# Kernel optimization log

Hardware: AMD Instinct MI355X
Metric: run time of the kernel (lower is better)

Reference implementation:

```python
import jax, jax.numpy as jnp
import numpy as np

B, L, C = 8, 4096, 256
H = 8            # num_heads
D = C // H       # head_dim = 32
CHUNK = 128


def _build_slopes(n):
    # ALiBi slopes for power-of-2 n: 2^(-8/n * (i+1)); cast fp16 like the torch module
    s = np.array([2.0 ** (-(8.0 / n) * (i + 1)) for i in range(n)], dtype=np.float32)
    return jnp.asarray(s.astype(np.float16).astype(np.float32))  # [H]


def setup_inputs() -> dict:
    key = jax.random.key(0)
    ks = jax.random.split(key, 6)
    x = jax.random.normal(ks[0], (B, L, C), dtype=jnp.float32)
    rel_pos = jax.random.normal(ks[1], (1, L, C), dtype=jnp.float32) * 0.02  # trunc_normal std=0.02
    qkv_w = jax.random.normal(ks[2], (3 * C, C), dtype=jnp.float32) * (C ** -0.5)
    q_gamma = jnp.ones((H, 1, D), dtype=jnp.float32) / (D ** 0.5)
    k_gamma = jnp.ones((H, 1, D), dtype=jnp.float32) / (D ** 0.5)
    proj_w = jax.random.normal(ks[3], (C, C), dtype=jnp.float32) * (C ** -0.5)
    proj_b = jnp.zeros((C,), dtype=jnp.float32)
    return {"x": x, "rel_pos": rel_pos, "qkv_w": qkv_w, "q_gamma": q_gamma,
            "k_gamma": k_gamma, "proj_w": proj_w, "proj_b": proj_b}


def _rms_norm(t, gamma):
    # t: [B,H,L,D]; gamma: [H,1,D]. F.normalize(dim=-1) then * sqrt(D) * gamma
    n = jnp.sqrt(jnp.sum(t * t, axis=-1, keepdims=True))
    t = t / jnp.maximum(n, 1e-12)
    return t * (D ** 0.5) * gamma[None]


def _lightning_attn(q, k, v, slopes):
    # q,k,v: [B,H,L,D]; slopes: [H]. o_t = sum_{s<=t} exp(-slope*(t-s)) (q_t.k_s) v_s
    nc = L // CHUNK
    c = CHUNK
    qc = q.reshape(B, H, nc, c, D)
    kc = k.reshape(B, H, nc, c, D)
    vc = v.reshape(B, H, nc, c, D)

    idx = jnp.arange(c, dtype=jnp.float32)
    diff = idx[:, None] - idx[None, :]                       # [c,c]
    s = slopes[:, None, None]                                # [H,1,1]
    mask = jnp.where(diff >= 0, jnp.exp(-s * diff), 0.0)     # [H,c,c]

    # intra-chunk: [B,H,nc,c,c]
    scores = jnp.einsum("bhncd,bhnmd->bhncm", qc, kc) * mask[None, :, None]
    o_intra = jnp.einsum("bhncm,bhnmd->bhncd", scores, vc)

    # inter-chunk recurrence over decayed KV state [B,H,D,D]
    q_decay = jnp.exp(-slopes[:, None] * idx[None, :])[None, :, :, None]        # [1,H,c,1]
    k_decay = jnp.exp(-slopes[:, None] * (c - idx[None, :]))[None, :, :, None]  # [1,H,c,1]
    blk_decay = jnp.exp(-slopes * c)[:, None, None]                             # [H,1,1]

    def step(kv, inp):
        qi, ki, vi = inp                                   # each [B,H,c,D]
        o = jnp.einsum("bhcd,bhde->bhce", qi * q_decay, kv)
        kv = blk_decay * kv + jnp.einsum("bhcd,bhce->bhde", ki * k_decay, vi)
        return kv, o

    kv0 = jnp.zeros((B, H, D, D), dtype=q.dtype)
    qs = jnp.moveaxis(qc, 2, 0)  # [nc,B,H,c,D]
    ks_ = jnp.moveaxis(kc, 2, 0)
    vs = jnp.moveaxis(vc, 2, 0)
    _, o_inter = jax.lax.scan(step, kv0, (qs, ks_, vs))    # [nc,B,H,c,D]
    o_inter = jnp.moveaxis(o_inter, 0, 2)                  # [B,H,nc,c,D]

    return (o_intra + o_inter).reshape(B, H, L, D)


def reference(x, rel_pos, qkv_w, q_gamma, k_gamma, proj_w, proj_b):
    slopes = _build_slopes(H)
    h = x + rel_pos                                        # [B,L,C]
    qkv = h @ qkv_w.T                                      # [B,L,3C]
    qkv = qkv.reshape(B, L, 3, H, D).transpose(2, 0, 3, 1, 4)  # [3,B,H,L,D]
    q, k, v = qkv[0], qkv[1], qkv[2]
    q = q * (D ** -0.5)            # no-op through normalize, kept for fidelity
    q = _rms_norm(q, q_gamma)
    k = _rms_norm(k, k_gamma)
    o = _lightning_attn(q, k, v, slopes)                   # [B,H,L,D]
    o = o.transpose(0, 2, 1, 3).reshape(B, L, C)
    return o @ proj_w.T + proj_b
```

## Files before the change

kernel.cpp:

```cpp
#include <hip/hip_runtime.h>
#include <hip/hip_bf16.h>

#define B_ 8
#define L_ 4096
#define C_ 256
#define H_ 8
#define D_ 32
#define CHUNK_ 128
#define NC_ 32
#define M_ (B_*L_)

typedef _Float16 f16x8 __attribute__((ext_vector_type(8)));
typedef _Float16 f16x4 __attribute__((ext_vector_type(4)));
typedef float    f32x4 __attribute__((ext_vector_type(4)));

#define GLOAD_LDS16(g, l) __builtin_amdgcn_global_load_lds( \
    (const __attribute__((address_space(1))) unsigned int*)(g), \
    (__attribute__((address_space(3))) unsigned int*)(l), 16, 0, 0)

__global__ __launch_bounds__(256) void k_cast_w(
    const float* __restrict__ qw, const float* __restrict__ pw,
    _Float16* __restrict__ qwb, _Float16* __restrict__ pwb)
{
    const int i = (blockIdx.x * 256 + threadIdx.x) * 4;
    const float* src; _Float16* dst; int off;
    if (i < 768 * 256) { src = qw; dst = qwb; off = i; }
    else               { src = pw; dst = pwb; off = i - 768 * 256; }
    float4 v = *(const float4*)(src + off);
    f16x4 o = { (_Float16)v.x, (_Float16)v.y, (_Float16)v.z, (_Float16)v.w };
    *(f16x4*)(dst + off) = o;
}

__global__ __launch_bounds__(512) void k_qkv_fused(
    const float* __restrict__ x, const float* __restrict__ rel,
    const _Float16* __restrict__ Bw,
    const float* __restrict__ qg, const float* __restrict__ kg,
    _Float16* __restrict__ Qg, _Float16* __restrict__ Kg, _Float16* __restrict__ Vtg)
{
    __shared__ __align__(16) char smem[24576];
    _Float16* As = (_Float16*)smem;
    _Float16* Bs = As + 128 * 32;
    _Float16* Ws = (_Float16*)smem;

    const int tid = threadIdx.x;
    const int wv = tid >> 6, ln = tid & 63;
    const int kind = blockIdx.x;
    const int m0 = blockIdx.y * 128;
    const int wr = wv >> 1, wc = wv & 1;
    const int lr = ln >> 2, lc = (ln & 3) * 8;
    const int fr = ln & 15, fk = (ln >> 4) * 8;

    const int arow = tid >> 2;
    const int aseg = (tid & 3) * 8;
    const float* xp = x   + (size_t)(m0 + arow) * 256 + aseg;
    const float* rp = rel + (size_t)((m0 + arow) & 4095) * 256 + aseg;
    const _Float16* gb = Bw + (size_t)(kind * 256 + wv * 16 + lr) * 256 + lc;

    f32x4 acc[2][8] = {};
    for (int k0 = 0; k0 < 256; k0 += 32) {
        GLOAD_LDS16(gb + k0,             Bs + (wv * 16) * 32);
        GLOAD_LDS16(gb + k0 + 128 * 256, Bs + (128 + wv * 16) * 32);
        float4 x0 = *(const float4*)(xp + k0);
        float4 x1 = *(const float4*)(xp + k0 + 4);
        float4 r0 = *(const float4*)(rp + k0);
        float4 r1 = *(const float4*)(rp + k0 + 4);
        f16x8 hv = { (_Float16)(x0.x + r0.x), (_Float16)(x0.y + r0.y),
                     (_Float16)(x0.z + r0.z), (_Float16)(x0.w + r0.w),
                     (_Float16)(x1.x + r1.x), (_Float16)(x1.y + r1.y),
                     (_Float16)(x1.z + r1.z), (_Float16)(x1.w + r1.w) };
        *(f16x8*)(As + arow * 32 + aseg) = hv;
        __syncthreads();
        f16x8 af[2], bf[8];
#pragma unroll
        for (int i = 0; i < 2; ++i)
            af[i] = *(const f16x8*)(As + (wr * 32 + i * 16 + fr) * 32 + fk);
#pragma unroll
        for (int j = 0; j < 8; ++j)
            bf[j] = *(const f16x8*)(Bs + (wc * 128 + j * 16 + fr) * 32 + fk);
#pragma unroll
        for (int i = 0; i < 2; ++i)
#pragma unroll
            for (int j = 0; j < 8; ++j)
                acc[i][j] = __builtin_amdgcn_mfma_f32_16x16x32_f16(
                    af[i], bf[j], acc[i][j], 0, 0, 0);
        __syncthreads();
    }

    const int cr = (ln >> 4) * 4, cc = ln & 15;
    const int bb = m0 >> 12, l00 = m0 & 4095;

    if (kind < 2) {
        const float* gsrc = kind ? kg : qg;
        _Float16* P = kind ? Kg : Qg;
#pragma unroll
        for (int p = 0; p < 4; ++p) {
            const int h = wc * 4 + p;
            const float g0 = gsrc[h * 32 + cc];
            const float g1 = gsrc[h * 32 + 16 + cc];
#pragma unroll
            for (int i = 0; i < 2; ++i)
#pragma unroll
                for (int r = 0; r < 4; ++r) {
                    const float a0 = acc[i][2 * p][r];
                    const float a1 = acc[i][2 * p + 1][r];
                    float ss = a0 * a0 + a1 * a1;
                    ss += __shfl_xor(ss, 1);
                    ss += __shfl_xor(ss, 2);
                    ss += __shfl_xor(ss, 4);
                    ss += __shfl_xor(ss, 8);
                    const float sc = 5.656854249492381f / fmaxf(sqrtf(ss), 1e-12f);
                    const int row = wr * 32 + i * 16 + cr + r;
                    Ws[row * 72 + wc * 32 + cc]      = (_Float16)(a0 * sc * g0);
                    Ws[row * 72 + wc * 32 + 16 + cc] = (_Float16)(a1 * sc * g1);
                }
            __syncthreads();
            const int half = tid >> 8;
            const int t = tid & 255;
            const int hh = half * 4 + p;
            _Float16* dst = P + ((size_t)(bb * 8 + hh) * 4096 + l00) * 32;
#pragma unroll
            for (int cidx = 0; cidx < 2; ++cidx) {
                const int c = t + cidx * 256;
                const int rr = c >> 2, part = (c & 3) * 8;
                f16x8 v8 = *(const f16x8*)(Ws + rr * 72 + half * 32 + part);
                *(f16x8*)(dst + rr * 32 + part) = v8;
            }
            __syncthreads();
        }
    } else {
#pragma unroll
        for (int i = 0; i < 2; ++i)
#pragma unroll
            for (int j = 0; j < 8; ++j) {
                const int col = wc * 128 + j * 16 + cc;
                const int hh = col >> 5, e = col & 31;
                const int l0 = l00 + wr * 32 + i * 16 + cr;
                f16x4 v4 = { (_Float16)acc[i][j][0], (_Float16)acc[i][j][1],
                             (_Float16)acc[i][j][2], (_Float16)acc[i][j][3] };
                *(f16x4*)(Vtg + ((size_t)(bb * 8 + hh) * 32 + e) * 4096 + l0) = v4;
            }
    }
}

__global__ __launch_bounds__(256) void k_chunk_kv(
    const _Float16* __restrict__ Kg, const _Float16* __restrict__ Vtg,
    float* __restrict__ kvbuf)
{
    __shared__ float ks[128 * 32];
    __shared__ float vs[128 * 36];
    const int blk = blockIdx.x;
    const int n  = blk & 31;
    const int bh = blk >> 5;
    const int h  = bh & 7;
    const float sl2 = exp2f(-(float)(h + 1)) * 1.44269504f;
    const int tid = threadIdx.x;
    const _Float16* Kc = Kg + ((size_t)bh * 4096 + n * CHUNK_) * 32;
#pragma unroll
    for (int i = 0; i < 2; ++i) {
        const int flat = i * 256 + tid;
        const int pos = flat >> 2, d0 = (flat & 3) * 8;
        f16x8 k8 = *(const f16x8*)(Kc + flat * 8);
        const float kd = exp2f(-sl2 * (float)(CHUNK_ - pos));
        f32x4 lo = { (float)k8[0] * kd, (float)k8[1] * kd, (float)k8[2] * kd, (float)k8[3] * kd };
        f32x4 hi = { (float)k8[4] * kd, (float)k8[5] * kd, (float)k8[6] * kd, (float)k8[7] * kd };
        *(f32x4*)&ks[pos * 32 + d0]     = lo;
        *(f32x4*)&ks[pos * 32 + d0 + 4] = hi;
        const int e = flat >> 4, seg = flat & 15;
        f16x8 v8 = *(const f16x8*)(Vtg + ((size_t)bh * 32 + e) * 4096 + n * CHUNK_ + seg * 8);
#pragma unroll
        for (int j = 0; j < 8; ++j) vs[(seg * 8 + j) * 36 + e] = (float)v8[j];
    }
    __syncthreads();
    const int d = tid >> 3;
    const int e0 = (tid & 7) * 4;
    f32x4 acc = {0.f, 0.f, 0.f, 0.f};
    for (int pos = 0; pos < CHUNK_; ++pos) {
        const float kd = ks[pos * 32 + d];
        f32x4 v4 = *(const f32x4*)&vs[pos * 36 + e0];
        acc += kd * v4;
    }
    *(f32x4*)(kvbuf + (size_t)blk * 1024 + d * 32 + e0) = acc;
}

__global__ __launch_bounds__(256) void k_scan(float* __restrict__ kvbuf)
{
    const int bh = blockIdx.x;
    const int tid = threadIdx.x;
    const float slope = exp2f(-(float)((bh & 7) + 1));
    const float bd = __expf(-slope * (float)CHUNK_);
    float4 st = {0.f, 0.f, 0.f, 0.f};
    float4* base = (float4*)(kvbuf + (size_t)bh * NC_ * 1024) + tid;
#pragma unroll
    for (int g = 0; g < 4; ++g) {
        float4 tmp[8];
#pragma unroll
        for (int k = 0; k < 8; ++k) tmp[k] = base[(g * 8 + k) * 256];
#pragma unroll
        for (int k = 0; k < 8; ++k) {
            base[(g * 8 + k) * 256] = st;
            st.x = bd * st.x + tmp[k].x;
            st.y = bd * st.y + tmp[k].y;
            st.z = bd * st.z + tmp[k].z;
            st.w = bd * st.w + tmp[k].w;
        }
    }
}

__global__ __launch_bounds__(256) void k_attn(
    const _Float16* __restrict__ Qg, const _Float16* __restrict__ Kg,
    const _Float16* __restrict__ Vtg, const float* __restrict__ kvbuf,
    _Float16* __restrict__ attnp)
{
    __shared__ _Float16 Qs[128 * 32];
    __shared__ _Float16 Ks[128 * 32];
    __shared__ _Float16 Vt[32 * 136];
    __shared__ _Float16 KVt[32 * 40];
    __shared__ _Float16 Ss[128 * 136];
    __shared__ _Float16 Os[128 * 36];
    __shared__ float ejs[CHUNK_];
    const int blk = blockIdx.x;
    const int n  = blk & 31;
    const int bh = blk >> 5;
    const int h  = bh & 7;
    const float sl2 = exp2f(-(float)(h + 1)) * 1.44269504f;
    const int tid = threadIdx.x;
    const int wv = tid >> 6, ln = tid & 63;

    const _Float16* Qc = Qg + ((size_t)bh * 4096 + n * CHUNK_) * 32;
    const _Float16* Kc = Kg + ((size_t)bh * 4096 + n * CHUNK_) * 32;
#pragma unroll
    for (int i = 0; i < 2; ++i) {
        GLOAD_LDS16(Qc + (wv * 128 + i * 64 + ln) * 8, Qs + (wv * 128 + i * 64) * 8);
        GLOAD_LDS16(Kc + (wv * 128 + i * 64 + ln) * 8, Ks + (wv * 128 + i * 64) * 8);
    }
#pragma unroll
    for (int i = 0; i < 2; ++i) {
        int flat = i * 256 + tid;
        int e = flat >> 4, seg = flat & 15;
        f16x8 v8 = *(const f16x8*)(Vtg + ((size_t)bh * 32 + e) * 4096 + n * CHUNK_ + seg * 8);
        *(f16x8*)(Vt + e * 136 + seg * 8) = v8;
    }
    {
        int e = tid & 31, dg = tid >> 5;
        const float* kvp = kvbuf + (size_t)blk * 1024;
        f16x4 kv4 = { (_Float16)kvp[(dg * 4 + 0) * 32 + e],
                      (_Float16)kvp[(dg * 4 + 1) * 32 + e],
                      (_Float16)kvp[(dg * 4 + 2) * 32 + e],
                      (_Float16)kvp[(dg * 4 + 3) * 32 + e] };
        *(f16x4*)(KVt + e * 40 + dg * 4) = kv4;
    }
    if (tid < CHUNK_) ejs[tid] = exp2f(sl2 * (float)tid);
    __syncthreads();

    const int fr = ln & 15, fk = (ln >> 4) * 8;
    const int cr = (ln >> 4) * 4, cc = ln & 15;

    f16x8 aq[2];
#pragma unroll
    for (int i = 0; i < 2; ++i)
        aq[i] = *(const f16x8*)(Qs + (wv * 32 + i * 16 + fr) * 32 + fk);

    f32x4 sacc[2][8] = {};
#pragma unroll
    for (int j = 0; j < 8; ++j) {
        f16x8 bk = *(const f16x8*)(Ks + (j * 16 + fr) * 32 + fk);
#pragma unroll
        for (int i = 0; i < 2; ++i)
            sacc[i][j] = __builtin_amdgcn_mfma_f32_16x16x32_f16(aq[i], bk, sacc[i][j], 0, 0, 0);
    }
    f32x4 iacc[2][2] = {};
#pragma unroll
    for (int ct = 0; ct < 2; ++ct) {
        f16x8 bkv = *(const f16x8*)(KVt + (ct * 16 + fr) * 40 + fk);
#pragma unroll
        for (int i = 0; i < 2; ++i)
            iacc[i][ct] = __builtin_amdgcn_mfma_f32_16x16x32_f16(aq[i], bkv, iacc[i][ct], 0, 0, 0);
    }
    float ejr[8];
#pragma unroll
    for (int j = 0; j < 8; ++j) ejr[j] = ejs[j * 16 + cc];
    const float c1 = exp2f(-sl2);
    float qd_save[2][4];
#pragma unroll
    for (int i = 0; i < 2; ++i) {
        float er = exp2f(-sl2 * (float)(wv * 32 + i * 16 + cr));
#pragma unroll
        for (int r = 0; r < 4; ++r) {
            const int irow = wv * 32 + i * 16 + cr + r;
            qd_save[i][r] = er;
#pragma unroll
            for (int j = 0; j < 8; ++j) {
                const int jcol = j * 16 + cc;
                const float w = (jcol <= irow) ? ejr[j] * er : 0.f;
                Ss[irow * 136 + jcol] = (_Float16)(sacc[i][j][r] * w);
            }
            er *= c1;
        }
    }
    __syncthreads();

    f32x4 oacc[2][2] = {};
#pragma unroll
    for (int k = 0; k < 4; ++k) {
        f16x8 as[2], bv[2];
#pragma unroll
        for (int i = 0; i < 2; ++i)
            as[i] = *(const f16x8*)(Ss + (wv * 32 + i * 16 + fr) * 136 + k * 32 + fk);
#pragma unroll
        for (int ct = 0; ct < 2; ++ct)
            bv[ct] = *(const f16x8*)(Vt + (ct * 16 + fr) * 136 + k * 32 + fk);
#pragma unroll
        for (int i = 0; i < 2; ++i)
#pragma unroll
            for (int ct = 0; ct < 2; ++ct)
                oacc[i][ct] = __builtin_amdgcn_mfma_f32_16x16x32_f16(as[i], bv[ct], oacc[i][ct], 0, 0, 0);
    }
#pragma unroll
    for (int i = 0; i < 2; ++i)
#pragma unroll
        for (int r = 0; r < 4; ++r) {
            const int irow = wv * 32 + i * 16 + cr + r;
            const float qd = qd_save[i][r];
            Os[irow * 36 + cc]      = (_Float16)(oacc[i][0][r] + qd * iacc[i][0][r]);
            Os[irow * 36 + 16 + cc] = (_Float16)(oacc[i][1][r] + qd * iacc[i][1][r]);
        }
    __syncthreads();
    _Float16* abase = attnp + ((size_t)bh * 4096 + n * CHUNK_) * 32;
#pragma unroll
    for (int kk = 0; kk < 2; ++kk) {
        const int c = kk * 256 + tid;
        const int rr = c >> 2;
        const int part = (c & 3) * 8;
        *(f16x8*)(abase + rr * 32 + part) = *(const f16x8*)(Os + rr * 36 + part);
    }
}

__global__ __launch_bounds__(256) void k_proj_gemm(
    const _Float16* __restrict__ attnp, const _Float16* __restrict__ Bw,
    const float* __restrict__ bias, float* __restrict__ Cc)
{
    __shared__ _Float16 As[128 * 32];
    __shared__ _Float16 Bs[128 * 32];
    const int tid = threadIdx.x;
    const int wv = tid >> 6, ln = tid & 63;
    const int m0 = blockIdx.y * 128;
    const int n0 = blockIdx.x * 128;
    const int lr = ln >> 2;
    const int lc = (ln & 3) * 8;
    const int wm = (wv >> 1) * 64;
    const int wn = (wv & 1) * 64;
    const int fr = ln & 15;
    const int fk = (ln >> 4) * 8;

    f32x4 acc[4][4] = {};
    const int gmrow = m0 + wv * 16 + lr;
    const _Float16* ga = attnp +
        ((size_t)(gmrow >> 12) * 8 * 4096 + (gmrow & 4095)) * 32 + lc;
    const _Float16* gb = Bw + (size_t)(n0 + wv * 16 + lr) * 256 + lc;

    for (int k0 = 0; k0 < 256; k0 += 32) {
        const size_t hoff = (size_t)(k0 >> 5) * (4096 * 32);
        GLOAD_LDS16(ga + hoff,           As + (wv * 16) * 32);
        GLOAD_LDS16(ga + hoff + 64 * 32, As + (64 + wv * 16) * 32);
        GLOAD_LDS16(gb + k0,             Bs + (wv * 16) * 32);
        GLOAD_LDS16(gb + k0 + 64 * 256,  Bs + (64 + wv * 16) * 32);
        __syncthreads();
        f16x8 af[4], bf[4];
#pragma unroll
        for (int i = 0; i < 4; ++i)
            af[i] = *(const f16x8*)(As + (wm + i * 16 + fr) * 32 + fk);
#pragma unroll
        for (int j = 0; j < 4; ++j)
            bf[j] = *(const f16x8*)(Bs + (wn + j * 16 + fr) * 32 + fk);
#pragma unroll
        for (int i = 0; i < 4; ++i)
#pragma unroll
            for (int j = 0; j < 4; ++j)
                acc[i][j] = __builtin_amdgcn_mfma_f32_16x16x32_f16(
                    af[i], bf[j], acc[i][j], 0, 0, 0);
        __syncthreads();
    }
    const int cr = (ln >> 4) * 4;
    const int cc = ln & 15;
#pragma unroll
    for (int i = 0; i < 4; ++i)
#pragma unroll
        for (int j = 0; j < 4; ++j) {
            const int row = m0 + wm + i * 16 + cr;
            const int col = n0 + wn + j * 16 + cc;
            float* cp = Cc + (size_t)row * 256 + col;
            const float bb = bias[col];
#pragma unroll
            for (int r = 0; r < 4; ++r) cp[(size_t)r * 256] = acc[i][j][r] + bb;
        }
}

extern "C" void kernel_launch(void* const* d_in, const int* in_sizes, int n_in,
                              void* d_out, int out_size, void* d_ws, size_t ws_size,
                              hipStream_t stream)
{
    const float* x     = (const float*)d_in[0];
    const float* rel   = (const float*)d_in[1];
    const float* qkv_w = (const float*)d_in[2];
    const float* qg    = (const float*)d_in[3];
    const float* kg    = (const float*)d_in[4];
    const float* pw    = (const float*)d_in[5];
    const float* pb    = (const float*)d_in[6];
    float* out = (float*)d_out;
    char* wsb = (char*)d_ws;

    float*    kvb   = (float*)wsb;
    _Float16* Qg    = (_Float16*)(wsb + ((size_t)8  << 20));
    _Float16* Kg    = (_Float16*)(wsb + ((size_t)24 << 20));
    _Float16* Vtg   = (_Float16*)(wsb + ((size_t)40 << 20));
    _Float16* attnp = (_Float16*)(wsb + ((size_t)56 << 20));
    _Float16* qwb   = (_Float16*)(wsb + ((size_t)72 << 20));
    _Float16* pwb   = (_Float16*)(wsb + ((size_t)73 << 20));

    k_cast_w<<<256, 256, 0, stream>>>(qkv_w, pw, qwb, pwb);
    k_qkv_fused<<<dim3(3, 256), 512, 0, stream>>>(x, rel, qwb, qg, kg, Qg, Kg, Vtg);
    k_chunk_kv<<<2048, 256, 0, stream>>>(Kg, Vtg, kvb);
    k_scan<<<64, 256, 0, stream>>>(kvb);
    k_attn<<<2048, 256, 0, stream>>>(Qg, Kg, Vtg, kvb, attnp);
    k_proj_gemm<<<dim3(2, 256), 256, 0, stream>>>(attnp, pwb, pb, out);
}
```

Baseline: 203.4 us.

## Split x+rel cast into own kernel, retile QKV GEMM, read attn operands from global

Result: faster. 188.3 us (-7.4%).

```diff
diff --git a/kernel.cpp b/kernel.cpp
--- a/kernel.cpp
+++ b/kernel.cpp
@@ -18,6 +18,22 @@
     (const __attribute__((address_space(1))) unsigned int*)(g), \
     (__attribute__((address_space(3))) unsigned int*)(l), 16, 0, 0)
 
+__global__ __launch_bounds__(256) void k_cast_h(
+    const float* __restrict__ x, const float* __restrict__ rel, _Float16* __restrict__ h)
+{
+    const int i = (blockIdx.x * 256 + threadIdx.x) * 8;
+    float4 x0 = *(const float4*)(x + i);
+    float4 x1 = *(const float4*)(x + i + 4);
+    const int ri = i & (L_ * C_ - 1);
+    float4 r0 = *(const float4*)(rel + ri);
+    float4 r1 = *(const float4*)(rel + ri + 4);
+    f16x8 o = { (_Float16)(x0.x + r0.x), (_Float16)(x0.y + r0.y),
+                (_Float16)(x0.z + r0.z), (_Float16)(x0.w + r0.w),
+                (_Float16)(x1.x + r1.x), (_Float16)(x1.y + r1.y),
+                (_Float16)(x1.z + r1.z), (_Float16)(x1.w + r1.w) };
+    *(f16x8*)(h + i) = o;
+}
+
 __global__ __launch_bounds__(256) void k_cast_w(
     const float* __restrict__ qw, const float* __restrict__ pw,
     _Float16* __restrict__ qwb, _Float16* __restrict__ pwb)
@@ -31,114 +47,116 @@
     *(f16x4*)(dst + off) = o;
 }
 
-__global__ __launch_bounds__(512) void k_qkv_fused(
-    const float* __restrict__ x, const float* __restrict__ rel,
-    const _Float16* __restrict__ Bw,
+__global__ __launch_bounds__(256) void k_qkv_gemm(
+    const _Float16* __restrict__ A, const _Float16* __restrict__ Bw,
     const float* __restrict__ qg, const float* __restrict__ kg,
     _Float16* __restrict__ Qg, _Float16* __restrict__ Kg, _Float16* __restrict__ Vtg)
 {
-    __shared__ __align__(16) char smem[24576];
+    __shared__ __align__(16) char smem[34816];
     _Float16* As = (_Float16*)smem;
     _Float16* Bs = As + 128 * 32;
     _Float16* Ws = (_Float16*)smem;
 
     const int tid = threadIdx.x;
     const int wv = tid >> 6, ln = tid & 63;
-    const int kind = blockIdx.x;
     const int m0 = blockIdx.y * 128;
-    const int wr = wv >> 1, wc = wv & 1;
+    const int n0 = blockIdx.x * 128;
     const int lr = ln >> 2, lc = (ln & 3) * 8;
+    const int wm = (wv >> 1) * 64, wn = (wv & 1) * 64;
     const int fr = ln & 15, fk = (ln >> 4) * 8;
 
-    const int arow = tid >> 2;
-    const int aseg = (tid & 3) * 8;
-    const float* xp = x   + (size_t)(m0 + arow) * 256 + aseg;
-    const float* rp = rel + (size_t)((m0 + arow) & 4095) * 256 + aseg;
-    const _Float16* gb = Bw + (size_t)(kind * 256 + wv * 16 + lr) * 256 + lc;
-
-    f32x4 acc[2][8] = {};
+    f32x4 acc[4][4] = {};
+    const _Float16* ga = A  + (size_t)(m0 + wv * 16 + lr) * 256 + lc;
+    const _Float16* gb = Bw + (size_t)(n0 + wv * 16 + lr) * 256 + lc;
+
     for (int k0 = 0; k0 < 256; k0 += 32) {
-        GLOAD_LDS16(gb + k0,             Bs + (wv * 16) * 32);
-        GLOAD_LDS16(gb + k0 + 128 * 256, Bs + (128 + wv * 16) * 32);
-        float4 x0 = *(const float4*)(xp + k0);
-        float4 x1 = *(const float4*)(xp + k0 + 4);
-        float4 r0 = *(const float4*)(rp + k0);
-        float4 r1 = *(const float4*)(rp + k0 + 4);
-        f16x8 hv = { (_Float16)(x0.x + r0.x), (_Float16)(x0.y + r0.y),
-                     (_Float16)(x0.z + r0.z), (_Float16)(x0.w + r0.w),
-                     (_Float16)(x1.x + r1.x), (_Float16)(x1.y + r1.y),
-                     (_Float16)(x1.z + r1.z), (_Float16)(x1.w + r1.w) };
-        *(f16x8*)(As + arow * 32 + aseg) = hv;
-        __syncthreads();
-        f16x8 af[2], bf[8];
-#pragma unroll
-        for (int i = 0; i < 2; ++i)
-            af[i] = *(const f16x8*)(As + (wr * 32 + i * 16 + fr) * 32 + fk);
-#pragma unroll
-        for (int j = 0; j < 8; ++j)
-            bf[j] = *(const f16x8*)(Bs + (wc * 128 + j * 16 + fr) * 32 + fk);
-#pragma unroll
-        for (int i = 0; i < 2; ++i)
-#pragma unroll
-            for (int j = 0; j < 8; ++j)
+        GLOAD_LDS16(ga + k0,            As + (wv * 16) * 32);
+        GLOAD_LDS16(ga + k0 + 64 * 256, As + (64 + wv * 16) * 32);
+        GLOAD_LDS16(gb + k0,            Bs + (wv * 16) * 32);
+        GLOAD_LDS16(gb + k0 + 64 * 256, Bs + (64 + wv * 16) * 32);
+        __syncthreads();
+        f16x8 af[4], bf[4];
+#pragma unroll
+        for (int i = 0; i < 4; ++i)
+            af[i] = *(const f16x8*)(As + (wm + i * 16 + fr) * 32 + fk);
+#pragma unroll
+        for (int j = 0; j < 4; ++j)
+            bf[j] = *(const f16x8*)(Bs + (wn + j * 16 + fr) * 32 + fk);
+#pragma unroll
+        for (int i = 0; i < 4; ++i)
+#pragma unroll
+            for (int j = 0; j < 4; ++j)
                 acc[i][j] = __builtin_amdgcn_mfma_f32_16x16x32_f16(
                     af[i], bf[j], acc[i][j], 0, 0, 0);
         __syncthreads();
     }
 
     const int cr = (ln >> 4) * 4, cc = ln & 15;
+    const int kind = n0 >> 8;
+    const int col0 = (n0 & 255) + wn;
     const int bb = m0 >> 12, l00 = m0 & 4095;
+    const int hbase = (n0 & 255) >> 5;
 
     if (kind < 2) {
         const float* gsrc = kind ? kg : qg;
-        _Float16* P = kind ? Kg : Qg;
-#pragma unroll
-        for (int p = 0; p < 4; ++p) {
-            const int h = wc * 4 + p;
-            const float g0 = gsrc[h * 32 + cc];
-            const float g1 = gsrc[h * 32 + 16 + cc];
-#pragma unroll
-            for (int i = 0; i < 2; ++i)
-#pragma unroll
-                for (int r = 0; r < 4; ++r) {
-                    const float a0 = acc[i][2 * p][r];
-                    const float a1 = acc[i][2 * p + 1][r];
+        float gma[2][2];
+#pragma unroll
+        for (int jp = 0; jp < 2; ++jp)
+#pragma unroll
+            for (int jj = 0; jj < 2; ++jj)
+                gma[jp][jj] = gsrc[((col0 >> 5) + jp) * 32 + jj * 16 + cc];
+#pragma unroll
+        for (int i = 0; i < 4; ++i)
+#pragma unroll
+            for (int r = 0; r < 4; ++r) {
+                const int irow = wm + i * 16 + cr + r;
+#pragma unroll
+                for (int jp = 0; jp < 2; ++jp) {
+                    const float a0 = acc[i][jp * 2][r];
+                    const float a1 = acc[i][jp * 2 + 1][r];
                     float ss = a0 * a0 + a1 * a1;
                     ss += __shfl_xor(ss, 1);
                     ss += __shfl_xor(ss, 2);
                     ss += __shfl_xor(ss, 4);
                     ss += __shfl_xor(ss, 8);
                     const float sc = 5.656854249492381f / fmaxf(sqrtf(ss), 1e-12f);
-                    const int row = wr * 32 + i * 16 + cr + r;
-                    Ws[row * 72 + wc * 32 + cc]      = (_Float16)(a0 * sc * g0);
-                    Ws[row * 72 + wc * 32 + 16 + cc] = (_Float16)(a1 * sc * g1);
+                    Ws[irow * 136 + wn + jp * 32 + cc]      = (_Float16)(a0 * sc * gma[jp][0]);
+                    Ws[irow * 136 + wn + jp * 32 + 16 + cc] = (_Float16)(a1 * sc * gma[jp][1]);
                 }
-            __syncthreads();
-            const int half = tid >> 8;
-            const int t = tid & 255;
-            const int hh = half * 4 + p;
-            _Float16* dst = P + ((size_t)(bb * 8 + hh) * 4096 + l00) * 32;
-#pragma unroll
-            for (int cidx = 0; cidx < 2; ++cidx) {
-                const int c = t + cidx * 256;
-                const int rr = c >> 2, part = (c & 3) * 8;
-                f16x8 v8 = *(const f16x8*)(Ws + rr * 72 + half * 32 + part);
-                *(f16x8*)(dst + rr * 32 + part) = v8;
             }
-            __syncthreads();
+        __syncthreads();
+        _Float16* P = kind ? Kg : Qg;
+#pragma unroll
+        for (int kk = 0; kk < 8; ++kk) {
+            const int c = kk * 256 + tid;
+            const int hh = c >> 9;
+            const int rr = (c >> 2) & 127;
+            const int part = (c & 3) * 8;
+            f16x8 v8 = *(const f16x8*)(Ws + rr * 136 + hh * 32 + part);
+            *(f16x8*)(P + ((size_t)(bb * 8 + hbase + hh) * 4096 + l00 + rr) * 32 + part) = v8;
         }
     } else {
 #pragma unroll
-        for (int i = 0; i < 2; ++i)
-#pragma unroll
-            for (int j = 0; j < 8; ++j) {
-                const int col = wc * 128 + j * 16 + cc;
-                const int hh = col >> 5, e = col & 31;
-                const int l0 = l00 + wr * 32 + i * 16 + cr;
+        for (int i = 0; i < 4; ++i)
+#pragma unroll
+            for (int j = 0; j < 4; ++j) {
+                const int colL = wn + j * 16 + cc;
+                const int row0 = wm + i * 16 + cr;
                 f16x4 v4 = { (_Float16)acc[i][j][0], (_Float16)acc[i][j][1],
                              (_Float16)acc[i][j][2], (_Float16)acc[i][j][3] };
-                *(f16x4*)(Vtg + ((size_t)(bb * 8 + hh) * 32 + e) * 4096 + l0) = v4;
+                *(f16x4*)(Ws + colL * 136 + row0) = v4;
             }
+        __syncthreads();
+#pragma unroll
+        for (int kk = 0; kk < 8; ++kk) {
+            const int q = kk * 256 + tid;
+            const int c = q >> 4;
+            const int seg = q & 15;
+            const int col = (n0 & 255) + c;
+            const int hh = col >> 5, e = col & 31;
+            f16x8 v8 = *(const f16x8*)(Ws + c * 136 + seg * 8);
+            *(f16x8*)(Vtg + ((size_t)(bb * 8 + hh) * 32 + e) * 4096 + l00 + seg * 8) = v8;
+        }
     }
 }
 
@@ -211,13 +229,10 @@
     const _Float16* __restrict__ Vtg, const float* __restrict__ kvbuf,
     _Float16* __restrict__ attnp)
 {
-    __shared__ _Float16 Qs[128 * 32];
-    __shared__ _Float16 Ks[128 * 32];
-    __shared__ _Float16 Vt[32 * 136];
-    __shared__ _Float16 KVt[32 * 40];
-    __shared__ _Float16 Ss[128 * 136];
-    __shared__ _Float16 Os[128 * 36];
+    __shared__ __align__(16) _Float16 Ss[128 * 136];
+    __shared__ __align__(16) _Float16 KVt[32 * 40];
     __shared__ float ejs[CHUNK_];
+    _Float16* Os = Ss;
     const int blk = blockIdx.x;
     const int n  = blk & 31;
     const int bh = blk >> 5;
@@ -225,23 +240,15 @@
     const float sl2 = exp2f(-(float)(h + 1)) * 1.44269504f;
     const int tid = threadIdx.x;
     const int wv = tid >> 6, ln = tid & 63;
+    const int fr = ln & 15, fk = (ln >> 4) * 8;
+    const int cr = (ln >> 4) * 4, cc = ln & 15;
 
     const _Float16* Qc = Qg + ((size_t)bh * 4096 + n * CHUNK_) * 32;
     const _Float16* Kc = Kg + ((size_t)bh * 4096 + n * CHUNK_) * 32;
-#pragma unroll
-    for (int i = 0; i < 2; ++i) {
-        GLOAD_LDS16(Qc + (wv * 128 + i * 64 + ln) * 8, Qs + (wv * 128 + i * 64) * 8);
-        GLOAD_LDS16(Kc + (wv * 128 + i * 64 + ln) * 8, Ks + (wv * 128 + i * 64) * 8);
-    }
-#pragma unroll
-    for (int i = 0; i < 2; ++i) {
-        int flat = i * 256 + tid;
-        int e = flat >> 4, seg = flat & 15;
-        f16x8 v8 = *(const f16x8*)(Vtg + ((size_t)bh * 32 + e) * 4096 + n * CHUNK_ + seg * 8);
-        *(f16x8*)(Vt + e * 136 + seg * 8) = v8;
-    }
+    const _Float16* Vc = Vtg + (size_t)bh * 32 * 4096 + n * CHUNK_;
+
     {
-        int e = tid & 31, dg = tid >> 5;
+        const int e = tid & 31, dg = tid >> 5;
         const float* kvp = kvbuf + (size_t)blk * 1024;
         f16x4 kv4 = { (_Float16)kvp[(dg * 4 + 0) * 32 + e],
                       (_Float16)kvp[(dg * 4 + 1) * 32 + e],
@@ -252,18 +259,15 @@
     if (tid < CHUNK_) ejs[tid] = exp2f(sl2 * (float)tid);
     __syncthreads();
 
-    const int fr = ln & 15, fk = (ln >> 4) * 8;
-    const int cr = (ln >> 4) * 4, cc = ln & 15;
-
     f16x8 aq[2];
 #pragma unroll
     for (int i = 0; i < 2; ++i)
-        aq[i] = *(const f16x8*)(Qs + (wv * 32 + i * 16 + fr) * 32 + fk);
+        aq[i] = *(const f16x8*)(Qc + (wv * 32 + i * 16 + fr) * 32 + fk);
 
     f32x4 sacc[2][8] = {};
 #pragma unroll
     for (int j = 0; j < 8; ++j) {
-        f16x8 bk = *(const f16x8*)(Ks + (j * 16 + fr) * 32 + fk);
+        f16x8 bk = *(const f16x8*)(Kc + (j * 16 + fr) * 32 + fk);
 #pragma unroll
         for (int i = 0; i < 2; ++i)
             sacc[i][j] = __builtin_amdgcn_mfma_f32_16x16x32_f16(aq[i], bk, sacc[i][j], 0, 0, 0);
@@ -308,21 +312,22 @@
             as[i] = *(const f16x8*)(Ss + (wv * 32 + i * 16 + fr) * 136 + k * 32 + fk);
 #pragma unroll
         for (int ct = 0; ct < 2; ++ct)
-            bv[ct] = *(const f16x8*)(Vt + (ct * 16 + fr) * 136 + k * 32 + fk);
+            bv[ct] = *(const f16x8*)(Vc + (size_t)(ct * 16 + fr) * 4096 + k * 32 + fk);
 #pragma unroll
         for (int i = 0; i < 2; ++i)
 #pragma unroll
             for (int ct = 0; ct < 2; ++ct)
                 oacc[i][ct] = __builtin_amdgcn_mfma_f32_16x16x32_f16(as[i], bv[ct], oacc[i][ct], 0, 0, 0);
     }
+    __syncthreads();
 #pragma unroll
     for (int i = 0; i < 2; ++i)
 #pragma unroll
         for (int r = 0; r < 4; ++r) {
             const int irow = wv * 32 + i * 16 + cr + r;
             const float qd = qd_save[i][r];
-            Os[irow * 36 + cc]      = (_Float16)(oacc[i][0][r] + qd * iacc[i][0][r]);
-            Os[irow * 36 + 16 + cc] = (_Float16)(oacc[i][1][r] + qd * iacc[i][1][r]);
+            Os[irow * 40 + cc]      = (_Float16)(oacc[i][0][r] + qd * iacc[i][0][r]);
+            Os[irow * 40 + 16 + cc] = (_Float16)(oacc[i][1][r] + qd * iacc[i][1][r]);
         }
     __syncthreads();
     _Float16* abase = attnp + ((size_t)bh * 4096 + n * CHUNK_) * 32;
@@ -331,7 +336,7 @@
         const int c = kk * 256 + tid;
         const int rr = c >> 2;
         const int part = (c & 3) * 8;
-        *(f16x8*)(abase + rr * 32 + part) = *(const f16x8*)(Os + rr * 36 + part);
+        *(f16x8*)(abase + rr * 32 + part) = *(const f16x8*)(Os + rr * 40 + part);
     }
 }
 
@@ -414,11 +419,13 @@
     _Float16* Kg    = (_Float16*)(wsb + ((size_t)24 << 20));
     _Float16* Vtg   = (_Float16*)(wsb + ((size_t)40 << 20));
     _Float16* attnp = (_Float16*)(wsb + ((size_t)56 << 20));
-    _Float16* qwb   = (_Float16*)(wsb + ((size_t)72 << 20));
-    _Float16* pwb   = (_Float16*)(wsb + ((size_t)73 << 20));
+    _Float16* hb    = (_Float16*)(wsb + ((size_t)72 << 20));
+    _Float16* qwb   = (_Float16*)(wsb + ((size_t)88 << 20));
+    _Float16* pwb   = (_Float16*)(wsb + ((size_t)89 << 20));
 
     k_cast_w<<<256, 256, 0, stream>>>(qkv_w, pw, qwb, pwb);
-    k_qkv_fused<<<dim3(3, 256), 512, 0, stream>>>(x, rel, qwb, qg, kg, Qg, Kg, Vtg);
+    k_cast_h<<<4096, 256, 0, stream>>>(x, rel, hb);
+    k_qkv_gemm<<<dim3(6, 256), 256, 0, stream>>>(hb, qwb, qg, kg, Qg, Kg, Vtg);
     k_chunk_kv<<<2048, 256, 0, stream>>>(Kg, Vtg, kvb);
     k_scan<<<64, 256, 0, stream>>>(kvb);
     k_attn<<<2048, 256, 0, stream>>>(Qg, Kg, Vtg, kvb, attnp);
```
